# Kernel tuning notes

Hardware: AMD Instinct MI355X
Metric: run time of the kernel (lower is better)

Reference implementation:

```python
import jax, jax.numpy as jnp
import numpy as np

H = 64  # hidden size hard-coded in the torch module


def _lstm_cell(x, h, c, Wih, Whh, b):
    # PyTorch LSTMCell: gates = x @ Wih.T + h @ Whh.T + bias_ih + bias_hh,
    # gate order (i, f, g, o), each of size H.
    gates = x @ Wih.T + h @ Whh.T + b
    i, f, g, o = jnp.split(gates, 4, axis=-1)
    c_new = jax.nn.sigmoid(f) * c + jax.nn.sigmoid(i) * jnp.tanh(g)
    h_new = jax.nn.sigmoid(o) * jnpp_tanh(c_new) if False else jax.nn.sigmoid(o) * jnp.tanh(c_new)
    return h_new, c_new


def setup_inputs() -> dict:
    key = jax.random.key(0)
    ks = jax.random.split(key, 12)
    B, T, F = 2048, 1024, 1
    s = 1.0 / np.sqrt(H)  # PyTorch LSTMCell/Linear init range

    def u(k, shape):
        return jax.random.uniform(k, shape, jnp.float32, -s, s)

    return {
        "input": jax.random.normal(ks[0], (B, T, F), jnp.float32),
        "Wih1": u(ks[1], (4 * H, F)),
        "Whh1": u(ks[2], (4 * H, H)),
        "bih1": u(ks[3], (4 * H,)),
        "bhh1": u(ks[4], (4 * H,)),
        "Wih2": u(ks[5], (4 * H, H)),
        "Whh2": u(ks[6], (4 * H, H)),
        "bih2": u(ks[7], (4 * H,)),
        "bhh2": u(ks[8], (4 * H,)),
        "Wl": u(ks[9], (1, H)),
        "bl": u(ks[10], (1,)),
        "future": 8,
    }


def reference(input, Wih1, Whh1, bih1, bhh1, Wih2, Whh2, bih2, bhh2, Wl, bl, future):
    B = input.shape[0]
    dtype = input.dtype
    z = jnp.zeros((B, H), dtype)
    b1 = bih1 + bhh1
    b2 = bih2 + bhh2

    def step(carry, x_t):
        h1, c1, h2, c2 = carry
        h1, c1 = _lstm_cell(x_t, h1, c1, Wih1, Whh1, b1)
        h2, c2 = _lstm_cell(h1, h2, c2, Wih2, Whh2, b2)
        return (h1, c1, h2, c2), None

    # scan over time: xs shaped [T, B, F]
    (h1, c1, h2, c2), _ = jax.lax.scan(step, (z, z, z, z), jnp.swapaxes(input, 0, 1))
    out = h2 @ Wl.T + bl  # readout from last input step

    def fstep(carry, _):
        out, h1, c1, h2, c2 = carry
        h1, c1 = _lstm_cell(out, h1, c1, Wih1, Whh1, b1)
        h2, c2 = _lstm_cell(h1, h2, c2, Wih2, Whh2, b2)
        out = h2 @ Wl.T + bl
        return (out, h1, c1, h2, c2), None

    (out, h1, c1, h2, c2), _ = jax.lax.scan(fstep, (out, h1, c1, h2, c2), None, length=future)
    return out[:, None, :]  # [B, 1, out_feature]
```

## Files before the change

### kernel.cpp

```cpp
#include <hip/hip_runtime.h>

#define HID 64
#define TSTEPS 1024
#define BPW 8
#define TW 512

typedef __attribute__((ext_vector_type(8))) short short8v;
typedef __attribute__((ext_vector_type(4))) float f32x4;

__device__ __forceinline__ unsigned short f2bf(float f) {
  unsigned u = __float_as_uint(f);
  u += 0x7FFFu + ((u >> 16) & 1u);
  return (unsigned short)(u >> 16);
}
__device__ __forceinline__ float bf2f(unsigned short h) {
  return __uint_as_float(((unsigned)h) << 16);
}
__device__ __forceinline__ float sigf(float x) {
  return __builtin_amdgcn_rcpf(1.0f + __expf(-x));
}
__device__ __forceinline__ float tanh_(float x) {
  return 1.0f - 2.0f * __builtin_amdgcn_rcpf(1.0f + __expf(2.0f * x));
}
__device__ __forceinline__ float dppror8(float x) {
  int xi = __float_as_int(x);
  int y = __builtin_amdgcn_update_dpp(xi, xi, 0x128, 0xF, 0xF, true);
  return __int_as_float(y);
}
__device__ __forceinline__ f32x4 mf(short8v a, short8v b, f32x4 c) {
  return __builtin_amdgcn_mfma_f32_16x16x32_bf16(a, b, c, 0, 0, 0);
}
__device__ __forceinline__ short8v ld_frag(const short* buf, int ss, int lane) {
  int byte = (ss * 64 + lane) * 16;
  byte ^= ((byte >> 7) & 7) << 4;
  return *(const short8v*)((const char*)buf + byte);
}
__device__ __forceinline__ void st_frag32(short* buf, int jj, int col, unsigned v) {
  int byte = (((jj >> 5) * 64 + ((jj & 31) >> 3) * 16 + col) * 8 + (jj & 7)) * 2;
  byte ^= ((byte >> 7) & 7) << 4;
  *(unsigned*)((char*)buf + byte) = v;
}
__device__ __forceinline__ void load8split(const float* rp, short8v& hi, short8v& lo) {
  float t[8];
#pragma unroll
  for (int e = 0; e < 8; ++e) t[e] = rp[e];
#pragma unroll
  for (int e = 0; e < 8; ++e) {
    unsigned short h = f2bf(t[e]);
    hi[e] = (short)h;
    lo[e] = (short)f2bf(t[e] - bf2f(h));
  }
}
__device__ __forceinline__ float cellup(float zi, float zf, float zg, float zo,
                                        float& c) {
  c = sigf(zf) * c + sigf(zi) * tanh_(zg);
  return sigf(zo) * tanh_(c);
}

struct __align__(128) SMem {
  float xin[TSTEPS + 1][BPW];
  short hf1[2][1024];
  short hf2[2][1024];
  float ro[4][BPW];
};

__global__ __launch_bounds__(TW, 2) void lstm2_kernel(
    const float* __restrict__ input, const float* __restrict__ Wih1,
    const float* __restrict__ Whh1, const float* __restrict__ bih1,
    const float* __restrict__ bhh1, const float* __restrict__ Wih2,
    const float* __restrict__ Whh2, const float* __restrict__ bih2,
    const float* __restrict__ bhh2, const float* __restrict__ Wl,
    const float* __restrict__ bl, const int* __restrict__ future,
    float* __restrict__ out) {
  __shared__ SMem s;
  const int tid = threadIdx.x;
  const int w = tid >> 6;
  const int lane = tid & 63;
  const int wq = w & 3;
  const int b = lane & 7;
  const int d = (lane >> 3) & 1;
  const int g = lane >> 4;
  const int j0 = 16 * wq + 4 * g + 2 * d;
  const int b0 = blockIdx.x * BPW;
  const bool isL1 = (w < 4);

  short8v WAh[4][2], WAl[4][2], WCh[4][2], WCl[4][2];
  const float* WCsrc = isL1 ? Whh1 : Wih2;
  const float* WAsrc = Whh2;
#pragma unroll
  for (int q = 0; q < 4; ++q) {
    const int m = (4 * q + wq) * 16 + (lane & 15);
    const int koff = (lane >> 4) * 8;
#pragma unroll
    for (int ss = 0; ss < 2; ++ss) {
      load8split(WCsrc + m * HID + ss * 32 + koff, WCh[q][ss], WCl[q][ss]);
      load8split(WAsrc + m * HID + ss * 32 + koff, WAh[q][ss], WAl[q][ss]);
    }
  }
#pragma unroll
  for (int q = 0; q < 4; ++q)
#pragma unroll
    for (int ss = 0; ss < 2; ++ss)
      asm volatile("" : "+v"(WAh[q][ss]), "+v"(WAl[q][ss]),
                        "+v"(WCh[q][ss]), "+v"(WCl[q][ss]));

  const float* biA = isL1 ? bih1 : bih2;
  const float* biB = isL1 ? bhh1 : bhh2;
  float bb[4][2], wi[4][2];
#pragma unroll
  for (int q = 0; q < 4; ++q)
#pragma unroll
    for (int i = 0; i < 2; ++i) {
      const int row = 64 * q + j0 + i;
      bb[q][i] = biA[row] + biB[row];
      wi[q][i] = isL1 ? Wih1[row] : 0.0f;
    }
  const float wl0 = isL1 ? 0.0f : Wl[j0];
  const float wl1 = isL1 ? 0.0f : Wl[j0 + 1];
  const float blv = bl[0];
  const int nfut = future[0];

  {
    const float* src = input + (size_t)b0 * TSTEPS;
    for (int idx = tid; idx < BPW * TSTEPS; idx += TW) {
      int bi = idx >> 10;
      int t = idx & (TSTEPS - 1);
      s.xin[t][bi] = src[idx];
    }
    for (int idx = tid; idx < 2 * 1024; idx += TW) {
      ((short*)s.hf1)[idx] = 0;
      ((short*)s.hf2)[idx] = 0;
    }
  }
  f32x4 acc[4];
#pragma unroll
  for (int q = 0; q < 4; ++q) acc[q] = (f32x4){0.f, 0.f, 0.f, 0.f};
  float cA = 0.f, cB = 0.f;
  float hn0 = 0.f, hn1 = 0.f;
  __syncthreads();

  const int total = TSTEPS + nfut;
  const f32x4 zf = (f32x4){0.f, 0.f, 0.f, 0.f};
  for (int sidx = 0; sidx < total; ++sidx) {
    const int p = sidx & 1, pn = p ^ 1;

    if (isL1) {
      float z0[4], z1[4];
#pragma unroll
      for (int q = 0; q < 4; ++q) {
        float s0 = acc[q][0] + dppror8(acc[q][0]);
        float s1 = acc[q][1] + dppror8(acc[q][1]);
        float s2 = acc[q][2] + dppror8(acc[q][2]);
        float s3 = acc[q][3] + dppror8(acc[q][3]);
        z0[q] = d ? s2 : s0;
        z1[q] = d ? s3 : s1;
      }
      const int xt = (sidx < TSTEPS) ? sidx : TSTEPS;
      const float xv = s.xin[xt][b];
#pragma unroll
      for (int q = 0; q < 4; ++q) {
        z0[q] += bb[q][0] + xv * wi[q][0];
        z1[q] += bb[q][1] + xv * wi[q][1];
      }
      float h0 = cellup(z0[0], z0[1], z0[2], z0[3], cA);
      float h1v = cellup(z1[0], z1[1], z1[2], z1[3], cB);
      unsigned short h0h = f2bf(h0), h1h = f2bf(h1v);
      unsigned short h0l = f2bf(h0 - bf2f(h0h));
      unsigned short h1l = f2bf(h1v - bf2f(h1h));
      st_frag32(s.hf1[pn], j0, b, (unsigned)h0h | ((unsigned)h1h << 16));
      st_frag32(s.hf1[pn], j0, b + 8, (unsigned)h0l | ((unsigned)h1l << 16));
    } else {
      short8v B0 = ld_frag(s.hf2[p], 0, lane);
      short8v B1 = ld_frag(s.hf2[p], 1, lane);
#pragma unroll
      for (int q = 0; q < 4; ++q)
        acc[q] = mf(WAh[q][1], B1,
                    mf(WAl[q][1], B1, mf(WAh[q][0], B0, mf(WAl[q][0], B0, zf))));
    }
    __syncthreads();

    {
      short8v B0 = ld_frag(s.hf1[pn], 0, lane);
      short8v B1 = ld_frag(s.hf1[pn], 1, lane);
      if (isL1) {
#pragma unroll
        for (int q = 0; q < 4; ++q)
          acc[q] = mf(WCh[q][1], B1,
                      mf(WCl[q][1], B1, mf(WCh[q][0], B0, mf(WCl[q][0], B0, zf))));
      } else {
#pragma unroll
        for (int q = 0; q < 4; ++q)
          acc[q] = mf(WCh[q][1], B1,
                      mf(WCl[q][1], B1,
                         mf(WCh[q][0], B0, mf(WCl[q][0], B0, acc[q]))));
        float z0[4], z1[4];
#pragma unroll
        for (int q = 0; q < 4; ++q) {
          float s0 = acc[q][0] + dppror8(acc[q][0]);
          float s1 = acc[q][1] + dppror8(acc[q][1]);
          float s2 = acc[q][2] + dppror8(acc[q][2]);
          float s3 = acc[q][3] + dppror8(acc[q][3]);
          z0[q] = (d ? s2 : s0) + bb[q][0];
          z1[q] = (d ? s3 : s1) + bb[q][1];
        }
        hn0 = cellup(z0[0], z0[1], z0[2], z0[3], cA);
        hn1 = cellup(z1[0], z1[1], z1[2], z1[3], cB);
        unsigned short h0h = f2bf(hn0), h1h = f2bf(hn1);
        unsigned short h0l = f2bf(hn0 - bf2f(h0h));
        unsigned short h1l = f2bf(hn1 - bf2f(h1h));
        st_frag32(s.hf2[pn], j0, b, (unsigned)h0h | ((unsigned)h1h << 16));
        st_frag32(s.hf2[pn], j0, b + 8, (unsigned)h0l | ((unsigned)h1l << 16));
      }
    }

    if (sidx >= TSTEPS - 1) {
      float v = isL1 ? 0.0f : (wl0 * hn0 + wl1 * hn1);
      v += __shfl_xor(v, 8, 64);
      v += __shfl_xor(v, 16, 64);
      v += __shfl_xor(v, 32, 64);
      if (!isL1 && lane < 8) s.ro[wq][lane] = v;
      __syncthreads();
      if (tid < 8)
        s.xin[TSTEPS][tid] =
            s.ro[0][tid] + s.ro[1][tid] + s.ro[2][tid] + s.ro[3][tid] + blv;
    }
    __syncthreads();
  }

  if (tid < 8) out[b0 + tid] = s.xin[TSTEPS][tid];
}

extern "C" void kernel_launch(void* const* d_in, const int* in_sizes, int n_in,
                              void* d_out, int out_size, void* d_ws,
                              size_t ws_size, hipStream_t stream) {
  const float* input = (const float*)d_in[0];
  const float* Wih1 = (const float*)d_in[1];
  const float* Whh1 = (const float*)d_in[2];
  const float* bih1 = (const float*)d_in[3];
  const float* bhh1 = (const float*)d_in[4];
  const float* Wih2 = (const float*)d_in[5];
  const float* Whh2 = (const float*)d_in[6];
  const float* bih2 = (const float*)d_in[7];
  const float* bhh2 = (const float*)d_in[8];
  const float* Wl = (const float*)d_in[9];
  const float* bl = (const float*)d_in[10];
  const int* fut = (const int*)d_in[11];
  float* out = (float*)d_out;

  const int B = in_sizes[0] / TSTEPS;
  const int blocks = B / BPW;

  hipLaunchKernelGGL(lstm2_kernel, dim3(blocks), dim3(TW), 0, stream, input,
                     Wih1, Whh1, bih1, bhh1, Wih2, Whh2, bih2, bhh2, Wl, bl,
                     fut, out);
}
```

Before: 923.1 us.

## Double block to 1024 threads, splitting each layer's gate rows across 8 waves

Doubles the workgroup from 512 to 1024 threads so each LSTM layer runs on 8 waves instead of 4. Each wave now owns two 16-row MFMA tiles instead of four, using a remapped weight-row permutation, and each lane updates one hidden unit instead of two. This shortens the serial per-step critical path of MFMA chains and cell updates. The cost is twice as many waves at every barrier, possibly lower occupancy under launch_bounds(1024,2), and 16-bit shared stores in place of 32-bit ones.

Result: no change. 929.2 us (+0.7%).

```diff
diff --git a/kernel.cpp b/kernel.cpp
--- a/kernel.cpp
+++ b/kernel.cpp
@@ -3,7 +3,7 @@
 #define HID 64
 #define TSTEPS 1024
 #define BPW 8
-#define TW 512
+#define TW 1024
 
 typedef __attribute__((ext_vector_type(8))) short short8v;
 typedef __attribute__((ext_vector_type(4))) float f32x4;
@@ -35,10 +35,10 @@
   byte ^= ((byte >> 7) & 7) << 4;
   return *(const short8v*)((const char*)buf + byte);
 }
-__device__ __forceinline__ void st_frag32(short* buf, int jj, int col, unsigned v) {
-  int byte = (((jj >> 5) * 64 + ((jj & 31) >> 3) * 16 + col) * 8 + (jj & 7)) * 2;
+__device__ __forceinline__ int frag_addr16(int j, int col) {
+  int byte = ((j >> 5) * 64 + ((j & 31) >> 3) * 16 + col) * 16 + (j & 7) * 2;
   byte ^= ((byte >> 7) & 7) << 4;
-  *(unsigned*)((char*)buf + byte) = v;
+  return byte;
 }
 __device__ __forceinline__ void load8split(const float* rp, short8v& hi, short8v& lo) {
   float t[8];
@@ -61,8 +61,10 @@
   float xin[TSTEPS + 1][BPW];
   short hf1[2][1024];
   short hf2[2][1024];
-  float ro[4][BPW];
+  float ro[8][BPW];
 };
+
+#define PINV(v) asm volatile("" : "+v"(v))
 
 __global__ __launch_bounds__(TW, 2) void lstm2_kernel(
     const float* __restrict__ input, const float* __restrict__ Wih1,
@@ -76,49 +78,51 @@
   const int tid = threadIdx.x;
   const int w = tid >> 6;
   const int lane = tid & 63;
-  const int wq = w & 3;
-  const int b = lane & 7;
-  const int d = (lane >> 3) & 1;
+  const int wv = w & 7;
+  const bool isL1 = (w < 8);
+  const int c = lane & 15;
+  const int b = c & 7;
+  const int d = (c >> 3) & 1;
   const int g = lane >> 4;
-  const int j0 = 16 * wq + 4 * g + 2 * d;
+  const int jl = 4 * (2 * wv + d) + g;
   const int b0 = blockIdx.x * BPW;
-  const bool isL1 = (w < 4);
-
-  short8v WAh[4][2], WAl[4][2], WCh[4][2], WCl[4][2];
+
+  short8v WAh[2][2], WAl[2][2], WCh[2][2], WCl[2][2];
   const float* WCsrc = isL1 ? Whh1 : Wih2;
-  const float* WAsrc = Whh2;
-#pragma unroll
-  for (int q = 0; q < 4; ++q) {
-    const int m = (4 * q + wq) * 16 + (lane & 15);
+#pragma unroll
+  for (int tt = 0; tt < 2; ++tt) {
+    const int T = 2 * wv + tt;
+    const int r16 = lane & 15;
+    const int m = 64 * (r16 & 3) + 4 * T + (r16 >> 2);
     const int koff = (lane >> 4) * 8;
 #pragma unroll
     for (int ss = 0; ss < 2; ++ss) {
-      load8split(WCsrc + m * HID + ss * 32 + koff, WCh[q][ss], WCl[q][ss]);
-      load8split(WAsrc + m * HID + ss * 32 + koff, WAh[q][ss], WAl[q][ss]);
-    }
-  }
-#pragma unroll
-  for (int q = 0; q < 4; ++q)
-#pragma unroll
-    for (int ss = 0; ss < 2; ++ss)
-      asm volatile("" : "+v"(WAh[q][ss]), "+v"(WAl[q][ss]),
-                        "+v"(WCh[q][ss]), "+v"(WCl[q][ss]));
+      load8split(WCsrc + m * HID + ss * 32 + koff, WCh[tt][ss], WCl[tt][ss]);
+      load8split(Whh2 + m * HID + ss * 32 + koff, WAh[tt][ss], WAl[tt][ss]);
+    }
+  }
+#pragma unroll
+  for (int tt = 0; tt < 2; ++tt)
+#pragma unroll
+    for (int ss = 0; ss < 2; ++ss) {
+      PINV(WAh[tt][ss]); PINV(WAl[tt][ss]);
+      PINV(WCh[tt][ss]); PINV(WCl[tt][ss]);
+    }
 
   const float* biA = isL1 ? bih1 : bih2;
   const float* biB = isL1 ? bhh1 : bhh2;
-  float bb[4][2], wi[4][2];
-#pragma unroll
-  for (int q = 0; q < 4; ++q)
-#pragma unroll
-    for (int i = 0; i < 2; ++i) {
-      const int row = 64 * q + j0 + i;
-      bb[q][i] = biA[row] + biB[row];
-      wi[q][i] = isL1 ? Wih1[row] : 0.0f;
-    }
-  const float wl0 = isL1 ? 0.0f : Wl[j0];
-  const float wl1 = isL1 ? 0.0f : Wl[j0 + 1];
+  float bb[4], wi[4];
+#pragma unroll
+  for (int q = 0; q < 4; ++q) {
+    const int row = 64 * q + jl;
+    bb[q] = biA[row] + biB[row];
+    wi[q] = isL1 ? Wih1[row] : 0.0f;
+  }
+  const float wlv = isL1 ? 0.0f : Wl[jl];
   const float blv = bl[0];
   const int nfut = future[0];
+  const int adr_hi = frag_addr16(jl, b);
+  const int adr_lo = frag_addr16(jl, b + 8);
 
   {
     const float* src = input + (size_t)b0 * TSTEPS;
@@ -132,97 +136,88 @@
       ((short*)s.hf2)[idx] = 0;
     }
   }
-  f32x4 acc[4];
-#pragma unroll
-  for (int q = 0; q < 4; ++q) acc[q] = (f32x4){0.f, 0.f, 0.f, 0.f};
-  float cA = 0.f, cB = 0.f;
-  float hn0 = 0.f, hn1 = 0.f;
+  const f32x4 zf = (f32x4){0.f, 0.f, 0.f, 0.f};
+  f32x4 acc0 = zf, acc1 = zf;
+  float cc = 0.f;
+  float hnew = 0.f;
   __syncthreads();
 
   const int total = TSTEPS + nfut;
-  const f32x4 zf = (f32x4){0.f, 0.f, 0.f, 0.f};
   for (int sidx = 0; sidx < total; ++sidx) {
     const int p = sidx & 1, pn = p ^ 1;
 
     if (isL1) {
-      float z0[4], z1[4];
+      float z[4];
 #pragma unroll
       for (int q = 0; q < 4; ++q) {
-        float s0 = acc[q][0] + dppror8(acc[q][0]);
-        float s1 = acc[q][1] + dppror8(acc[q][1]);
-        float s2 = acc[q][2] + dppror8(acc[q][2]);
-        float s3 = acc[q][3] + dppror8(acc[q][3]);
-        z0[q] = d ? s2 : s0;
-        z1[q] = d ? s3 : s1;
+        float z0 = acc0[q] + dppror8(acc0[q]);
+        float z1 = acc1[q] + dppror8(acc1[q]);
+        z[q] = d ? z1 : z0;
       }
       const int xt = (sidx < TSTEPS) ? sidx : TSTEPS;
       const float xv = s.xin[xt][b];
 #pragma unroll
-      for (int q = 0; q < 4; ++q) {
-        z0[q] += bb[q][0] + xv * wi[q][0];
-        z1[q] += bb[q][1] + xv * wi[q][1];
-      }
-      float h0 = cellup(z0[0], z0[1], z0[2], z0[3], cA);
-      float h1v = cellup(z1[0], z1[1], z1[2], z1[3], cB);
-      unsigned short h0h = f2bf(h0), h1h = f2bf(h1v);
-      unsigned short h0l = f2bf(h0 - bf2f(h0h));
-      unsigned short h1l = f2bf(h1v - bf2f(h1h));
-      st_frag32(s.hf1[pn], j0, b, (unsigned)h0h | ((unsigned)h1h << 16));
-      st_frag32(s.hf1[pn], j0, b + 8, (unsigned)h0l | ((unsigned)h1l << 16));
+      for (int q = 0; q < 4; ++q) z[q] += bb[q] + xv * wi[q];
+      hnew = cellup(z[0], z[1], z[2], z[3], cc);
+      unsigned short hh = f2bf(hnew);
+      unsigned short hl = f2bf(hnew - bf2f(hh));
+      char* hf1w = (char*)s.hf1[pn];
+      *(short*)(hf1w + adr_hi) = (short)hh;
+      *(short*)(hf1w + adr_lo) = (short)hl;
     } else {
       short8v B0 = ld_frag(s.hf2[p], 0, lane);
       short8v B1 = ld_frag(s.hf2[p], 1, lane);
-#pragma unroll
-      for (int q = 0; q < 4; ++q)
-        acc[q] = mf(WAh[q][1], B1,
-                    mf(WAl[q][1], B1, mf(WAh[q][0], B0, mf(WAl[q][0], B0, zf))));
+      acc0 = mf(WAh[0][1], B1,
+                mf(WAl[0][1], B1, mf(WAh[0][0], B0, mf(WAl[0][0], B0, zf))));
+      acc1 = mf(WAh[1][1], B1,
+                mf(WAl[1][1], B1, mf(WAh[1][0], B0, mf(WAl[1][0], B0, zf))));
     }
     __syncthreads();
 
     {
-      short8v B0 = ld_frag(s.hf1[pn], 0, lane);
-      short8v B1 = ld_frag(s.hf1[pn], 1, lane);
+      short8v C0 = ld_frag(s.hf1[pn], 0, lane);
+      short8v C1 = ld_frag(s.hf1[pn], 1, lane);
       if (isL1) {
-#pragma unroll
-        for (int q = 0; q < 4; ++q)
-          acc[q] = mf(WCh[q][1], B1,
-                      mf(WCl[q][1], B1, mf(WCh[q][0], B0, mf(WCl[q][0], B0, zf))));
+        acc0 = mf(WCh[0][1], C1,
+                  mf(WCl[0][1], C1, mf(WCh[0][0], C0, mf(WCl[0][0], C0, zf))));
+        acc1 = mf(WCh[1][1], C1,
+                  mf(WCl[1][1], C1, mf(WCh[1][0], C0, mf(WCl[1][0], C0, zf))));
       } else {
-#pragma unroll
-        for (int q = 0; q < 4; ++q)
-          acc[q] = mf(WCh[q][1], B1,
-                      mf(WCl[q][1], B1,
-                         mf(WCh[q][0], B0, mf(WCl[q][0], B0, acc[q]))));
-        float z0[4], z1[4];
+        acc0 = mf(WCh[0][1], C1,
+                  mf(WCl[0][1], C1, mf(WCh[0][0], C0, mf(WCl[0][0], C0, acc0))));
+        acc1 = mf(WCh[1][1], C1,
+                  mf(WCl[1][1], C1, mf(WCh[1][0], C0, mf(WCl[1][0], C0, acc1))));
+        float z[4];
 #pragma unroll
         for (int q = 0; q < 4; ++q) {
-          float s0 = acc[q][0] + dppror8(acc[q][0]);
-          float s1 = acc[q][1] + dppror8(acc[q][1]);
-          float s2 = acc[q][2] + dppror8(acc[q][2]);
-          float s3 = acc[q][3] + dppror8(acc[q][3]);
-          z0[q] = (d ? s2 : s0) + bb[q][0];
-          z1[q] = (d ? s3 : s1) + bb[q][1];
+          float z0 = acc0[q] + dppror8(acc0[q]);
+          float z1 = acc1[q] + dppror8(acc1[q]);
+          z[q] = (d ? z1 : z0) + bb[q];
         }
-        hn0 = cellup(z0[0], z0[1], z0[2], z0[3], cA);
-        hn1 = cellup(z1[0], z1[1], z1[2], z1[3], cB);
-        unsigned short h0h = f2bf(hn0), h1h = f2bf(hn1);
-        unsigned short h0l = f2bf(hn0 - bf2f(h0h));
-        unsigned short h1l = f2bf(hn1 - bf2f(h1h));
-        st_frag32(s.hf2[pn], j0, b, (unsigned)h0h | ((unsigned)h1h << 16));
-        st_frag32(s.hf2[pn], j0, b + 8, (unsigned)h0l | ((unsigned)h1l << 16));
+        hnew = cellup(z[0], z[1], z[2], z[3], cc);
+        unsigned short hh = f2bf(hnew);
+        unsigned short hl = f2bf(hnew - bf2f(hh));
+        char* hf2w = (char*)s.hf2[pn];
+        *(short*)(hf2w + adr_hi) = (short)hh;
+        *(short*)(hf2w + adr_lo) = (short)hl;
       }
     }
 
     if (sidx >= TSTEPS - 1) {
-      float v = isL1 ? 0.0f : (wl0 * hn0 + wl1 * hn1);
-      v += __shfl_xor(v, 8, 64);
-      v += __shfl_xor(v, 16, 64);
-      v += __shfl_xor(v, 32, 64);
-      if (!isL1 && lane < 8) s.ro[wq][lane] = v;
+      if (!isL1) {
+        float v = wlv * hnew;
+        v += __shfl_xor(v, 8, 64);
+        v += __shfl_xor(v, 16, 64);
+        v += __shfl_xor(v, 32, 64);
+        if (lane < 8) s.ro[wv][lane] = v;
+      }
       __syncthreads();
-      if (tid < 8)
-        s.xin[TSTEPS][tid] =
-            s.ro[0][tid] + s.ro[1][tid] + s.ro[2][tid] + s.ro[3][tid] + blv;
+      if (tid < 8) {
+        float t = blv;
+#pragma unroll
+        for (int k = 0; k < 8; ++k) t += s.ro[k][tid];
+        s.xin[TSTEPS][tid] = t;
+      }
     }
     __syncthreads();
   }
```
